# Kernel tuning notes

Measured on AMD Instinct MI355X. Metric: run time of the kernel, lower is better.

## Reference

```python
import jax, jax.numpy as jnp
import numpy as np

N = 20000
E = 320000
IN_C, HID, OUT_C = 128, 64, 32
H12, H3 = 4, 1  # heads for conv1/conv2 and conv3
NEG_SLOPE = 0.2


def _glorot(key, shape):
    fan_in, fan_out = shape[0], shape[-1]
    lim = (6.0 / (fan_in + fan_out)) ** 0.5
    return jax.random.uniform(key, shape, jnp.float32, -lim, lim)


def setup_inputs() -> dict:
    key = jax.random.key(0)
    ks = jax.random.split(key, 16)
    x = jax.random.normal(ks[0], (N, IN_C), jnp.float32)
    edge_index = jax.random.randint(ks[1], (2, E), 0, N, jnp.int64)
    p = {
        'W1': _glorot(ks[2], (IN_C, H12 * HID)),
        'as1': _glorot(ks[3], (H12, HID)), 'ad1': _glorot(ks[4], (H12, HID)),
        'b1': jnp.zeros((HID,), jnp.float32),
        'W2': _glorot(ks[5], (HID, H12 * HID)),
        'as2': _glorot(ks[6], (H12, HID)), 'ad2': _glorot(ks[7], (H12, HID)),
        'b2': jnp.zeros((HID,), jnp.float32),
        'W3': _glorot(ks[8], (HID, H3 * OUT_C)),
        'as3': _glorot(ks[9], (H3, OUT_C)), 'ad3': _glorot(ks[10], (H3, OUT_C)),
        'b3': jnp.zeros((OUT_C,), jnp.float32),
        'Wm': _glorot(ks[11], (OUT_C, OUT_C)), 'bm': jnp.zeros((OUT_C,), jnp.float32),
        'Wv': _glorot(ks[12], (OUT_C, OUT_C)), 'bv': jnp.zeros((OUT_C,), jnp.float32),
    }
    return dict(x=x, edge_index=edge_index, **p)


def gat_layer(x, src, dst, W, a_src, a_dst, b, heads, out_c):
    # x: [N, in_c] -> h: [N, H, C]
    h = (x @ W).reshape(-1, heads, out_c)
    alpha_s = jnp.einsum('nhc,hc->nh', h, a_src)  # [N,H]
    alpha_d = jnp.einsum('nhc,hc->nh', h, a_dst)
    e = jax.nn.leaky_relu(alpha_s[src] + alpha_d[dst], NEG_SLOPE)  # [E',H]
    # segment softmax over incoming edges of each dst node
    m = jax.ops.segment_max(e, dst, num_segments=N)
    p = jnp.exp(e - m[dst])
    s = jax.ops.segment_sum(p, dst, num_segments=N)
    alpha = p / (s[dst] + 1e-16)  # [E',H]
    msg = h[src] * alpha[:, :, None]  # [E',H,C]
    out = jax.ops.segment_sum(msg, dst, num_segments=N)  # [N,H,C]
    return out.mean(axis=1) + b  # concat=False -> mean over heads


def reference(x, edge_index, W1, as1, ad1, b1, W2, as2, ad2, b2,
              W3, as3, ad3, b3, Wm, bm, Wv, bv):
    # PyG GATConv default: add self loops
    loop = jnp.arange(N, dtype=edge_index.dtype)
    src = jnp.concatenate([edge_index[0], loop])
    dst = jnp.concatenate([edge_index[1], loop])

    h = jax.nn.relu(gat_layer(x, src, dst, W1, as1, ad1, b1, H12, HID))
    h = jax.nn.relu(gat_layer(h, src, dst, W2, as2, ad2, b2, H12, HID))
    z = gat_layer(h, src, dst, W3, as3, ad3, b3, H3, OUT_C)

    z_mean = z @ Wm + bm
    z_var = jnp.clip(jnp.exp(z @ Wv + bv), 1e-8, 100.0)
    return (z_mean, z_var, z)
```

## Files before the change

### kernel.cpp

```cpp
#include <hip/hip_runtime.h>
#include <hip/hip_bf16.h>

typedef unsigned short ushortT;
typedef short short8 __attribute__((ext_vector_type(8)));
typedef unsigned short ushort8v __attribute__((ext_vector_type(8)));
typedef float float4v __attribute__((ext_vector_type(4)));

constexpr int Nn   = 20000;
constexpr int Ee   = 320000;
constexpr int EP   = Ee + Nn;
constexpr float NSL = 0.2f;
constexpr int CAP  = 128;

__device__ __forceinline__ float b2f(__hip_bfloat16 v) { return __bfloat162float(v); }
__device__ __forceinline__ float bits2f(unsigned short u) {
    __hip_bfloat16 b; *(unsigned short*)&b = u; return __bfloat162float(b);
}
__device__ __forceinline__ unsigned short f2bits(float v) {
    __hip_bfloat16 b = __float2bfloat16(v); return *(unsigned short*)&b;
}
__device__ __forceinline__ float ldf(const void* p, size_t i, int bf) {
    return bf ? __bfloat162float(((const __hip_bfloat16*)p)[i])
              : ((const float*)p)[i];
}
__device__ __forceinline__ void stf(void* p, size_t i, float v, int bf) {
    if (bf) ((__hip_bfloat16*)p)[i] = __float2bfloat16(v);
    else    ((float*)p)[i] = v;
}

__device__ __forceinline__ int local_bf(const unsigned* __restrict__ xbits, int* c_sh) {
    int c = 0;
    for (int i = threadIdx.x; i < 512; i += 256) {
        unsigned e = (xbits[i] >> 7) & 0xFFu;
        if (e >= 110u && e <= 135u) ++c;
    }
    atomicAdd(c_sh, c);
    __syncthreads();
    return (*c_sh > 384) ? 1 : 0;
}

__global__ void setup_k(const int* __restrict__ ei, const unsigned* __restrict__ xbits,
                        int* __restrict__ eflag, int* __restrict__ fflag,
                        int* __restrict__ cnt,
                        const void* __restrict__ W1, const void* __restrict__ W2,
                        const void* __restrict__ as1, const void* __restrict__ ad1,
                        const void* __restrict__ as2, const void* __restrict__ ad2,
                        ushortT* __restrict__ WT1c, ushortT* __restrict__ WT2c,
                        float* __restrict__ wp1, float* __restrict__ wp2) {
    const int b = blockIdx.x;
    if (b < 79) {
        int gi = b * 256 + threadIdx.x;
        if (gi < Nn) cnt[gi] = 0;
        if (b == 0) {
            __shared__ int bad, c_s;
            if (threadIdx.x == 0) { bad = 0; c_s = 0; }
            __syncthreads();
            for (int i = threadIdx.x; i < 1024; i += 256)
                if (ei[2 * i + 1] != 0) bad = 1;
            int bf = local_bf(xbits, &c_s);
            __syncthreads();
            if (threadIdx.x == 0) {
                *eflag = bad ? 0 : 1;
                *fflag = bf;
            }
        }
        return;
    }
    __shared__ int c_s;
    if (threadIdx.x == 0) c_s = 0;
    __syncthreads();
    const int bf = local_bf(xbits, &c_s);
    if (b < 271) {
        int idx = (b - 79) * 256 + threadIdx.x;
        if (idx < 64 * 512) {
            int jp = idx >> 9, r = idx & 511, hh = r >> 7, k = r & 127;
            WT1c[idx] = f2bits(ldf(W1, (size_t)k * 256 + hh * 64 + jp, bf));
        } else {
            int i2 = idx - 64 * 512;
            int jp = i2 >> 8, r = i2 & 255, hh = r >> 6, k = r & 63;
            WT2c[i2] = f2bits(ldf(W2, (size_t)k * 256 + hh * 64 + jp, bf));
        }
    } else {
        int idx = (b - 271) * 256 + threadIdx.x;
        if (idx < 1024) {
            int sd = idx >> 9, r = idx & 511, hh = r >> 7, k = r & 127;
            const void* av = sd ? ad1 : as1;
            float acc = 0.f;
            for (int c = 0; c < 64; ++c)
                acc = fmaf(ldf(W1, (size_t)k * 256 + hh * 64 + c, bf),
                           ldf(av, hh * 64 + c, bf), acc);
            wp1[idx] = acc;
        } else if (idx < 1536) {
            int i2 = idx - 1024;
            int sd = i2 >> 8, r = i2 & 255, hh = r >> 6, k = r & 63;
            const void* av = sd ? ad2 : as2;
            float acc = 0.f;
            for (int c = 0; c < 64; ++c)
                acc = fmaf(ldf(W2, (size_t)k * 256 + hh * 64 + c, bf),
                           ldf(av, hh * 64 + c, bf), acc);
            wp2[i2] = acc;
        }
    }
}

__device__ __forceinline__ void load_edge(const int* __restrict__ ei, int sh, int e,
                                          int& si, int& di) {
    if (e < Ee) {
        si = ei[(size_t)e << sh];
        di = ei[(size_t)(Ee + e) << sh];
    } else {
        si = di = e - Ee;
    }
}

__global__ void scatter_k(const int* __restrict__ ei, const int* __restrict__ eflag,
                          int* __restrict__ cnt, int* __restrict__ csr) {
    int e = blockIdx.x * 256 + threadIdx.x;
    if (e >= EP) return;
    int sh = *eflag, si, di;
    load_edge(ei, sh, e, si, di);
    int pos = atomicAdd(cnt + di, 1);
    if (pos < CAP) csr[di * CAP + pos] = si;
}

__global__ __launch_bounds__(256) void alpha1_k(const void* __restrict__ xg,
                                                const float* __restrict__ wp1,
                                                ushortT* __restrict__ xb,
                                                float* __restrict__ as_,
                                                float* __restrict__ ad_,
                                                const int* __restrict__ fflag, int N) {
    const int bf = *fflag;
    const int cl = threadIdx.x & 31, g = threadIdx.x >> 5;
    const int n = blockIdx.x * 8 + g;
    if (n >= N) return;
    const int c4 = cl * 4;
    float xv[4];
    if (bf) {
        ushort4 u = *(const ushort4*)((const ushortT*)xg + (size_t)n * 128 + c4);
        xv[0] = bits2f(u.x); xv[1] = bits2f(u.y); xv[2] = bits2f(u.z); xv[3] = bits2f(u.w);
        *(ushort4*)(xb + (size_t)n * 128 + c4) = u;
    } else {
        float4 f = *(const float4*)((const float*)xg + (size_t)n * 128 + c4);
        xv[0] = f.x; xv[1] = f.y; xv[2] = f.z; xv[3] = f.w;
        ushort4 u;
        u.x = f2bits(f.x); u.y = f2bits(f.y); u.z = f2bits(f.z); u.w = f2bits(f.w);
        *(ushort4*)(xb + (size_t)n * 128 + c4) = u;
    }
    float p[8];
#pragma unroll
    for (int j = 0; j < 8; ++j) {
        float4 wv = *(const float4*)(wp1 + j * 128 + c4);
        float t = 0.f;
        t = fmaf(xv[0], wv.x, t);
        t = fmaf(xv[1], wv.y, t);
        t = fmaf(xv[2], wv.z, t);
        t = fmaf(xv[3], wv.w, t);
        p[j] = t;
    }
#pragma unroll
    for (int off = 1; off < 32; off <<= 1) {
#pragma unroll
        for (int j = 0; j < 8; ++j) p[j] += __shfl_xor(p[j], off, 32);
    }
    if (cl == 0) {
        *(float4*)(as_ + (size_t)n * 4) = make_float4(p[0], p[1], p[2], p[3]);
        *(float4*)(ad_ + (size_t)n * 4) = make_float4(p[4], p[5], p[6], p[7]);
    }
}

template <int CIN>
__global__ __launch_bounds__(256) void aggx_k(const int* __restrict__ cnt,
                                              const int* __restrict__ csr,
                                              const float* __restrict__ as_,
                                              const float* __restrict__ ad_,
                                              const ushortT* __restrict__ xb,
                                              ushortT* __restrict__ aggn, int N) {
    constexpr int LPE = CIN / 8;
    constexpr int EPW = 64 / LPE;
    __shared__ float lal[4][CAP][4];
    const int lane = threadIdx.x & 63, seg = threadIdx.x >> 6;
    int d = blockIdx.x * 4 + seg;
    if (d >= N) d = N - 1;
    const int deg = min(cnt[d], CAP);
    const int base = d * CAP;
    const float4 adv = *(const float4*)(ad_ + d * 4);
    const int src0 = (lane < deg) ? csr[base + lane] : 0;
    const int src1 = (64 + lane < deg) ? csr[base + 64 + lane] : 0;
    float s0 = 0, s1 = 0, s2 = 0, s3 = 0;
    if (lane < deg) {
        float4 av = *(const float4*)(as_ + src0 * 4);
        float v0 = av.x + adv.x; v0 = v0 > 0.f ? v0 : NSL * v0; float e0 = __expf(v0);
        float v1 = av.y + adv.y; v1 = v1 > 0.f ? v1 : NSL * v1; float e1 = __expf(v1);
        float v2 = av.z + adv.z; v2 = v2 > 0.f ? v2 : NSL * v2; float e2 = __expf(v2);
        float v3 = av.w + adv.w; v3 = v3 > 0.f ? v3 : NSL * v3; float e3 = __expf(v3);
        s0 += e0; s1 += e1; s2 += e2; s3 += e3;
        *(float4*)(&lal[seg][lane][0]) = make_float4(e0, e1, e2, e3);
    }
    if (64 + lane < deg) {
        float4 av = *(const float4*)(as_ + src1 * 4);
        float v0 = av.x + adv.x; v0 = v0 > 0.f ? v0 : NSL * v0; float e0 = __expf(v0);
        float v1 = av.y + adv.y; v1 = v1 > 0.f ? v1 : NSL * v1; float e1 = __expf(v1);
        float v2 = av.z + adv.z; v2 = v2 > 0.f ? v2 : NSL * v2; float e2 = __expf(v2);
        float v3 = av.w + adv.w; v3 = v3 > 0.f ? v3 : NSL * v3; float e3 = __expf(v3);
        s0 += e0; s1 += e1; s2 += e2; s3 += e3;
        *(float4*)(&lal[seg][64 + lane][0]) = make_float4(e0, e1, e2, e3);
    }
    const int EL = lane / LPE;
    const int c8 = (lane & (LPE - 1)) * 8;
    const float* lal_s = &lal[seg][0][0];
    float a[4][8];
#pragma unroll
    for (int h = 0; h < 4; ++h)
#pragma unroll
        for (int j = 0; j < 8; ++j) a[h][j] = 0.f;

    auto do_edge = [&](int idx, bool valid) {
        int sa = __shfl(src0, idx & 63, 64);
        int sb = __shfl(src1, idx & 63, 64);
        int src = (idx < 64) ? sa : sb;
        int ii = valid ? idx : 0;
        float4 ev = *(const float4*)(lal_s + ii * 4);
        float g = valid ? 1.f : 0.f;
        int off = valid ? src * CIN : 0;
        ushort8v xv = *(const ushort8v*)(xb + (size_t)off + c8);
        float ex0 = ev.x * g, ex1 = ev.y * g, ex2 = ev.z * g, ex3 = ev.w * g;
#pragma unroll
        for (int j = 0; j < 8; ++j) {
            float xf = bits2f(xv[j]);
            a[0][j] = fmaf(ex0, xf, a[0][j]);
            a[1][j] = fmaf(ex1, xf, a[1][j]);
            a[2][j] = fmaf(ex2, xf, a[2][j]);
            a[3][j] = fmaf(ex3, xf, a[3][j]);
        }
    };

    int e = 0;
    for (; e + 2 * EPW <= deg; e += 2 * EPW) {
        do_edge(e + EL, true);
        do_edge(e + EPW + EL, true);
    }
    for (; e < deg; e += EPW) do_edge(e + EL, (e + EL) < deg);

#pragma unroll
    for (int off = 1; off < 64; off <<= 1) {
        s0 += __shfl_xor(s0, off, 64);
        s1 += __shfl_xor(s1, off, 64);
        s2 += __shfl_xor(s2, off, 64);
        s3 += __shfl_xor(s3, off, 64);
    }
#pragma unroll
    for (int h = 0; h < 4; ++h)
#pragma unroll
        for (int j = 0; j < 8; ++j) {
#pragma unroll
            for (int off2 = LPE; off2 < 64; off2 <<= 1)
                a[h][j] += __shfl_xor(a[h][j], off2, 64);
        }
    if (EL == 0) {
        const float i0 = 0.25f / (s0 + 1e-16f);
        const float i1 = 0.25f / (s1 + 1e-16f);
        const float i2 = 0.25f / (s2 + 1e-16f);
        const float i3 = 0.25f / (s3 + 1e-16f);
        ushortT* op = aggn + (size_t)d * (4 * CIN) + c8;
        ushort8v p0, p1, p2, p3;
#pragma unroll
        for (int j = 0; j < 8; ++j) {
            p0[j] = f2bits(a[0][j] * i0);
            p1[j] = f2bits(a[1][j] * i1);
            p2[j] = f2bits(a[2][j] * i2);
            p3[j] = f2bits(a[3][j] * i3);
        }
        *(ushort8v*)(op + 0 * CIN) = p0;
        *(ushort8v*)(op + 1 * CIN) = p1;
        *(ushort8v*)(op + 2 * CIN) = p2;
        *(ushort8v*)(op + 3 * CIN) = p3;
    }
}

template <int K, int NPROJ>
__global__ __launch_bounds__(256) void gemm_cat(const ushortT* __restrict__ aggn,
                                                const ushortT* __restrict__ WTc,
                                                const void* __restrict__ bias,
                                                const float* __restrict__ wp,
                                                ushortT* __restrict__ xout,
                                                float* __restrict__ as_,
                                                float* __restrict__ ad_,
                                                const int* __restrict__ fflag, int N) {
    constexpr int KC = 128, SW = KC + 8, NCH = K / KC;
    const int bf = *fflag;
    __shared__ ushortT wt_s[64 * SW];
    __shared__ ushortT xs[64 * SW];
    __shared__ float wp_s[512];
    const int base = blockIdx.x * 64;
    const int lane = threadIdx.x & 63, w = threadIdx.x >> 6;
    const int ln = lane & 15, quad = lane >> 4;
    float4v acc[4];
#pragma unroll
    for (int T = 0; T < 4; ++T) acc[T] = (float4v){0.f, 0.f, 0.f, 0.f};
    if (NPROJ) {
        for (int i = threadIdx.x; i < NPROJ * 64; i += 256) wp_s[i] = wp[i];
    }
#pragma unroll
    for (int ch = 0; ch < NCH; ++ch) {
        for (int i = threadIdx.x; i < 64 * 16; i += 256) {
            int r = i >> 4, kc = (i & 15) * 8;
            *(short8*)(wt_s + r * SW + kc) =
                *(const short8*)(WTc + (size_t)r * K + ch * KC + kc);
            int node = base + r;
            short8 v = {0, 0, 0, 0, 0, 0, 0, 0};
            if (node < N) v = *(const short8*)(aggn + (size_t)node * K + ch * KC + kc);
            *(short8*)(xs + r * SW + kc) = v;
        }
        __syncthreads();
#pragma unroll
        for (int ks = 0; ks < 4; ++ks) {
            const int kb = ks * 32 + quad * 8;
            const short8 bfr = *(const short8*)(xs + (w * 16 + ln) * SW + kb);
#pragma unroll
            for (int T = 0; T < 4; ++T) {
                const short8 afr = *(const short8*)(wt_s + (T * 16 + ln) * SW + kb);
                acc[T] = __builtin_amdgcn_mfma_f32_16x16x32_bf16(afr, bfr, acc[T], 0, 0, 0);
            }
        }
        __syncthreads();
    }
    const int node = base + w * 16 + ln;
    const bool live = node < N;
    ushortT* on = xout + (size_t)node * 64;
    float p[8];
#pragma unroll
    for (int j = 0; j < 8; ++j) p[j] = 0.f;
#pragma unroll
    for (int T = 0; T < 4; ++T) {
        const int jl = T * 16 + quad * 4;
        ushort4 pk;
        float t0 = fmaxf(acc[T][0] + ldf(bias, jl + 0, bf), 0.f);
        float t1 = fmaxf(acc[T][1] + ldf(bias, jl + 1, bf), 0.f);
        float t2 = fmaxf(acc[T][2] + ldf(bias, jl + 2, bf), 0.f);
        float t3 = fmaxf(acc[T][3] + ldf(bias, jl + 3, bf), 0.f);
        pk.x = f2bits(t0); pk.y = f2bits(t1); pk.z = f2bits(t2); pk.w = f2bits(t3);
        if (live) *(ushort4*)(on + jl) = pk;
        if (NPROJ) {
#pragma unroll
            for (int j = 0; j < 8; ++j) {
                p[j] = fmaf(t0, wp_s[j * 64 + jl + 0], p[j]);
                p[j] = fmaf(t1, wp_s[j * 64 + jl + 1], p[j]);
                p[j] = fmaf(t2, wp_s[j * 64 + jl + 2], p[j]);
                p[j] = fmaf(t3, wp_s[j * 64 + jl + 3], p[j]);
            }
        }
    }
    if (NPROJ) {
#pragma unroll
        for (int j = 0; j < 8; ++j) {
            p[j] += __shfl_xor(p[j], 16, 64);
            p[j] += __shfl_xor(p[j], 32, 64);
        }
        if (quad == 0 && live) {
            *(float4*)(as_ + (size_t)node * 4) = make_float4(p[0], p[1], p[2], p[3]);
            *(float4*)(ad_ + (size_t)node * 4) = make_float4(p[4], p[5], p[6], p[7]);
        }
    }
}

__global__ __launch_bounds__(256) void gemm_small(const ushortT* __restrict__ x,
                                                  const void* __restrict__ W,
                                                  __hip_bfloat16* __restrict__ h,
                                                  const void* __restrict__ avs,
                                                  const void* __restrict__ avd,
                                                  float* __restrict__ as_, float* __restrict__ ad_,
                                                  const int* __restrict__ fflag, int N) {
    constexpr int INC = 64, R = 32, PAD = R + 4;
    const int bf = *fflag;
    __shared__ float xsh[INC * PAD];
    int base = blockIdx.x * R;
    for (int i = threadIdx.x; i < R * INC; i += 256) {
        int rr = i / INC, kk = i - rr * INC;
        int nn = base + rr;
        xsh[kk * PAD + rr] = (nn < N) ? bits2f(x[(size_t)nn * INC + kk]) : 0.0f;
    }
    __syncthreads();
    const int jc = threadIdx.x & 31;
    const int g  = threadIdx.x >> 5;
    float acc[4] = {};
    if (bf) {
        const __hip_bfloat16* Wb = (const __hip_bfloat16*)W;
#pragma unroll 4
        for (int k = 0; k < INC; ++k) {
            float4 xv = *(const float4*)(xsh + k * PAD + g * 4);
            float w = b2f(Wb[k * 32 + jc]);
            acc[0] = fmaf(xv.x, w, acc[0]);
            acc[1] = fmaf(xv.y, w, acc[1]);
            acc[2] = fmaf(xv.z, w, acc[2]);
            acc[3] = fmaf(xv.w, w, acc[3]);
        }
    } else {
        const float* Wf = (const float*)W;
#pragma unroll 4
        for (int k = 0; k < INC; ++k) {
            float4 xv = *(const float4*)(xsh + k * PAD + g * 4);
            float w = Wf[k * 32 + jc];
            acc[0] = fmaf(xv.x, w, acc[0]);
            acc[1] = fmaf(xv.y, w, acc[1]);
            acc[2] = fmaf(xv.z, w, acc[2]);
            acc[3] = fmaf(xv.w, w, acc[3]);
        }
    }
    float avsr = ldf(avs, jc, bf), avdr = ldf(avd, jc, bf);
#pragma unroll
    for (int m = 0; m < 4; ++m) {
        int n = base + g * 4 + m;
        if (n >= N) continue;
        h[(size_t)n * 32 + jc] = __float2bfloat16(acc[m]);
        float t1 = acc[m] * avsr;
        float t2 = acc[m] * avdr;
#pragma unroll
        for (int off = 16; off > 0; off >>= 1) {
            t1 += __shfl_down(t1, off, 32);
            t2 += __shfl_down(t2, off, 32);
        }
        if (jc == 0) { as_[n] = t1; ad_[n] = t2; }
    }
}

__global__ __launch_bounds__(256) void aggr1f_k(const int* __restrict__ cnt,
                                                const int* __restrict__ csr,
                                                const float* __restrict__ as_,
                                                const float* __restrict__ ad_,
                                                const ushortT* __restrict__ h,
                                                const void* __restrict__ b3,
                                                const void* __restrict__ Wm,
                                                const void* __restrict__ bm,
                                                const void* __restrict__ Wv,
                                                const void* __restrict__ bv,
                                                const int* __restrict__ fflag,
                                                void* __restrict__ out, int N) {
    __shared__ float wm_s[1024], wv_s[1024];
    __shared__ float lal[8][CAP];
    __shared__ int   lof[8][CAP];
    const int bf = *fflag;
    for (int i = threadIdx.x; i < 1024; i += 256) {
        wm_s[i] = ldf(Wm, i, bf);
        wv_s[i] = ldf(Wv, i, bf);
    }
    __syncthreads();
    const int c = threadIdx.x & 31, seg = threadIdx.x >> 5;
    const int d = blockIdx.x * 8 + seg;
    if (d >= N) return;
    const int deg = min(cnt[d], CAP);
    const int base = d * CAP;
    const float advd = ad_[d];
    float s = 0;
    for (int i = c; i < deg; i += 32) {
        int src = csr[base + i];
        float v = as_[src] + advd;
        v = v > 0.f ? v : NSL * v;
        float ev = __expf(v);
        s += ev;
        lal[seg][i] = ev;
        lof[seg][i] = src * 32;
    }
    float acc = 0.0f;
    int e = 0;
    for (; e + 4 <= deg; e += 4) {
        float ev0 = lal[seg][e], ev1 = lal[seg][e + 1];
        float ev2 = lal[seg][e + 2], ev3 = lal[seg][e + 3];
        int o0 = lof[seg][e], o1 = lof[seg][e + 1];
        int o2 = lof[seg][e + 2], o3 = lof[seg][e + 3];
        float h0 = bits2f(h[o0 + c]), h1 = bits2f(h[o1 + c]);
        float h2 = bits2f(h[o2 + c]), h3 = bits2f(h[o3 + c]);
        acc = fmaf(ev0, h0, acc);
        acc = fmaf(ev1, h1, acc);
        acc = fmaf(ev2, h2, acc);
        acc = fmaf(ev3, h3, acc);
    }
    for (; e < deg; ++e) acc = fmaf(lal[seg][e], bits2f(h[lof[seg][e] + c]), acc);
#pragma unroll
    for (int off = 1; off < 32; off <<= 1) s += __shfl_xor(s, off, 32);
    const float inv = 1.0f / (s + 1e-16f);
    const float z = inv * acc + ldf(b3, c, bf);
    stf(out, (size_t)2 * N * 32 + (size_t)d * 32 + c, z, bf);
    float sm = ldf(bm, c, bf), sv = ldf(bv, c, bf);
#pragma unroll 8
    for (int k = 0; k < 32; ++k) {
        float zk = __shfl(z, k, 32);
        sm = fmaf(zk, wm_s[k * 32 + c], sm);
        sv = fmaf(zk, wv_s[k * 32 + c], sv);
    }
    float var = __expf(sv);
    var = fminf(fmaxf(var, 1e-8f), 100.0f);
    stf(out, (size_t)d * 32 + c, sm, bf);
    stf(out, (size_t)N * 32 + (size_t)d * 32 + c, var, bf);
}

extern "C" void kernel_launch(void* const* d_in, const int* in_sizes, int n_in,
                              void* d_out, int out_size, void* d_ws, size_t ws_size,
                              hipStream_t stream) {
    const void* x   = d_in[0];
    const int*  ei  = (const int*)d_in[1];
    const void* W1  = d_in[2];
    const void* as1 = d_in[3];
    const void* ad1 = d_in[4];
    const void* b1  = d_in[5];
    const void* W2  = d_in[6];
    const void* as2 = d_in[7];
    const void* ad2 = d_in[8];
    const void* b2  = d_in[9];
    const void* W3  = d_in[10];
    const void* as3 = d_in[11];
    const void* ad3 = d_in[12];
    const void* b3  = d_in[13];
    const void* Wm  = d_in[14];
    const void* bm  = d_in[15];
    const void* Wv  = d_in[16];
    const void* bv  = d_in[17];

    float* ws = (float*)d_ws;
    ushortT* aggn = (ushortT*)ws;
    ushortT* xb   = (ushortT*)(ws + 5120000);
    ushortT* x1b  = (ushortT*)(ws + 6400000);
    ushortT* x2b  = (ushortT*)(ws + 7040000);
    ushortT* h3   = (ushortT*)(ws + 7680000);
    float*  as_   = ws + 8000000;
    float*  ad_   = ws + 8080000;
    ushortT* WT1c = (ushortT*)(ws + 8160000);
    ushortT* WT2c = (ushortT*)(ws + 8176384);
    float*  wp1   = ws + 8184576;
    float*  wp2   = ws + 8185600;
    int*    cnt   = (int*)(ws + 8186112);
    int*    csr   = (int*)(ws + 8206112);
    int*    eflag = (int*)(ws + 10766112);
    int*    fflag = (int*)(ws + 10766113);

    setup_k<<<277, 256, 0, stream>>>(ei, (const unsigned*)x, eflag, fflag, cnt,
                                     W1, W2, as1, ad1, as2, ad2, WT1c, WT2c, wp1, wp2);
    scatter_k<<<(EP + 255) / 256, 256, 0, stream>>>(ei, eflag, cnt, csr);

    alpha1_k<<<2500, 256, 0, stream>>>(x, wp1, xb, as_, ad_, fflag, Nn);
    aggx_k<128><<<5000, 256, 0, stream>>>(cnt, csr, as_, ad_, xb, aggn, Nn);
    gemm_cat<512, 8><<<313, 256, 0, stream>>>(aggn, WT1c, b1, wp2, x1b, as_, ad_, fflag, Nn);

    aggx_k<64><<<5000, 256, 0, stream>>>(cnt, csr, as_, ad_, x1b, aggn, Nn);
    gemm_cat<256, 0><<<313, 256, 0, stream>>>(aggn, WT2c, b2, nullptr, x2b, as_, ad_, fflag, Nn);

    gemm_small<<<625, 256, 0, stream>>>(x2b, W3, (__hip_bfloat16*)h3, as3, ad3, as_, ad_, fflag, Nn);
    aggr1f_k<<<2500, 256, 0, stream>>>(cnt, csr, as_, ad_, h3,
                                       b3, Wm, bm, Wv, bv, fflag, d_out, Nn);
}
```

Measured before the change: 243.1 us.

## Split heads across lanes in aggregation kernels to drop cross-lane reductions

The aggregation kernels now map lanes to (head, channel chunk) instead of (edge, channel chunk). Each lane handles one head, so it keeps 8 accumulators instead of 32 and the large butterfly shuffle reduction over edges disappears (the 64-channel variant still needs one shuffle). The cost is that every lane walks the edges serially, and gathered rows are loaded redundantly by the four head groups, which hurts memory-level parallelism on the per-node loop.

```diff
diff --git a/kernel.cpp b/kernel.cpp
--- a/kernel.cpp
+++ b/kernel.cpp
@@ -168,15 +168,12 @@
     }
 }
 
-template <int CIN>
-__global__ __launch_bounds__(256) void aggx_k(const int* __restrict__ cnt,
-                                              const int* __restrict__ csr,
-                                              const float* __restrict__ as_,
-                                              const float* __restrict__ ad_,
-                                              const ushortT* __restrict__ xb,
-                                              ushortT* __restrict__ aggn, int N) {
-    constexpr int LPE = CIN / 8;
-    constexpr int EPW = 64 / LPE;
+__global__ __launch_bounds__(256) void aggx128_k(const int* __restrict__ cnt,
+                                                 const int* __restrict__ csr,
+                                                 const float* __restrict__ as_,
+                                                 const float* __restrict__ ad_,
+                                                 const ushortT* __restrict__ xb,
+                                                 ushortT* __restrict__ aggn, int N) {
     __shared__ float lal[4][CAP][4];
     const int lane = threadIdx.x & 63, seg = threadIdx.x >> 6;
     int d = blockIdx.x * 4 + seg;
@@ -205,41 +202,28 @@
         s0 += e0; s1 += e1; s2 += e2; s3 += e3;
         *(float4*)(&lal[seg][64 + lane][0]) = make_float4(e0, e1, e2, e3);
     }
-    const int EL = lane / LPE;
-    const int c8 = (lane & (LPE - 1)) * 8;
+    const int q = lane >> 4, c8 = (lane & 15) * 8;
     const float* lal_s = &lal[seg][0][0];
-    float a[4][8];
-#pragma unroll
-    for (int h = 0; h < 4; ++h)
-#pragma unroll
-        for (int j = 0; j < 8; ++j) a[h][j] = 0.f;
-
-    auto do_edge = [&](int idx, bool valid) {
+    float a[8] = {0, 0, 0, 0, 0, 0, 0, 0};
+
+    auto do_edge = [&](int idx) {
         int sa = __shfl(src0, idx & 63, 64);
         int sb = __shfl(src1, idx & 63, 64);
         int src = (idx < 64) ? sa : sb;
-        int ii = valid ? idx : 0;
-        float4 ev = *(const float4*)(lal_s + ii * 4);
-        float g = valid ? 1.f : 0.f;
-        int off = valid ? src * CIN : 0;
-        ushort8v xv = *(const ushort8v*)(xb + (size_t)off + c8);
-        float ex0 = ev.x * g, ex1 = ev.y * g, ex2 = ev.z * g, ex3 = ev.w * g;
-#pragma unroll
-        for (int j = 0; j < 8; ++j) {
-            float xf = bits2f(xv[j]);
-            a[0][j] = fmaf(ex0, xf, a[0][j]);
-            a[1][j] = fmaf(ex1, xf, a[1][j]);
-            a[2][j] = fmaf(ex2, xf, a[2][j]);
-            a[3][j] = fmaf(ex3, xf, a[3][j]);
-        }
+        float ev = lal_s[idx * 4 + q];
+        ushort8v xv = *(const ushort8v*)(xb + (size_t)src * 128 + c8);
+#pragma unroll
+        for (int j = 0; j < 8; ++j) a[j] = fmaf(ev, bits2f(xv[j]), a[j]);
     };
 
     int e = 0;
-    for (; e + 2 * EPW <= deg; e += 2 * EPW) {
-        do_edge(e + EL, true);
-        do_edge(e + EPW + EL, true);
-    }
-    for (; e < deg; e += EPW) do_edge(e + EL, (e + EL) < deg);
+    for (; e + 4 <= deg; e += 4) {
+        do_edge(e);
+        do_edge(e + 1);
+        do_edge(e + 2);
+        do_edge(e + 3);
+    }
+    for (; e < deg; ++e) do_edge(e);
 
 #pragma unroll
     for (int off = 1; off < 64; off <<= 1) {
@@ -248,32 +232,89 @@
         s2 += __shfl_xor(s2, off, 64);
         s3 += __shfl_xor(s3, off, 64);
     }
-#pragma unroll
-    for (int h = 0; h < 4; ++h)
-#pragma unroll
-        for (int j = 0; j < 8; ++j) {
-#pragma unroll
-            for (int off2 = LPE; off2 < 64; off2 <<= 1)
-                a[h][j] += __shfl_xor(a[h][j], off2, 64);
-        }
-    if (EL == 0) {
-        const float i0 = 0.25f / (s0 + 1e-16f);
-        const float i1 = 0.25f / (s1 + 1e-16f);
-        const float i2 = 0.25f / (s2 + 1e-16f);
-        const float i3 = 0.25f / (s3 + 1e-16f);
-        ushortT* op = aggn + (size_t)d * (4 * CIN) + c8;
-        ushort8v p0, p1, p2, p3;
-#pragma unroll
-        for (int j = 0; j < 8; ++j) {
-            p0[j] = f2bits(a[0][j] * i0);
-            p1[j] = f2bits(a[1][j] * i1);
-            p2[j] = f2bits(a[2][j] * i2);
-            p3[j] = f2bits(a[3][j] * i3);
-        }
-        *(ushort8v*)(op + 0 * CIN) = p0;
-        *(ushort8v*)(op + 1 * CIN) = p1;
-        *(ushort8v*)(op + 2 * CIN) = p2;
-        *(ushort8v*)(op + 3 * CIN) = p3;
+    const float sq = (q == 0) ? s0 : (q == 1) ? s1 : (q == 2) ? s2 : s3;
+    const float iq = 0.25f / (sq + 1e-16f);
+    ushort8v p;
+#pragma unroll
+    for (int j = 0; j < 8; ++j) p[j] = f2bits(a[j] * iq);
+    *(ushort8v*)(aggn + (size_t)d * 512 + q * 128 + c8) = p;
+}
+
+__global__ __launch_bounds__(256) void aggx64_k(const int* __restrict__ cnt,
+                                                const int* __restrict__ csr,
+                                                const float* __restrict__ as_,
+                                                const float* __restrict__ ad_,
+                                                const ushortT* __restrict__ xb,
+                                                ushortT* __restrict__ aggn, int N) {
+    __shared__ float lal[4][CAP][4];
+    const int lane = threadIdx.x & 63, seg = threadIdx.x >> 6;
+    int d = blockIdx.x * 4 + seg;
+    if (d >= N) d = N - 1;
+    const int deg = min(cnt[d], CAP);
+    const int base = d * CAP;
+    const float4 adv = *(const float4*)(ad_ + d * 4);
+    const int src0 = (lane < deg) ? csr[base + lane] : 0;
+    const int src1 = (64 + lane < deg) ? csr[base + 64 + lane] : 0;
+    float s0 = 0, s1 = 0, s2 = 0, s3 = 0;
+    if (lane < deg) {
+        float4 av = *(const float4*)(as_ + src0 * 4);
+        float v0 = av.x + adv.x; v0 = v0 > 0.f ? v0 : NSL * v0; float e0 = __expf(v0);
+        float v1 = av.y + adv.y; v1 = v1 > 0.f ? v1 : NSL * v1; float e1 = __expf(v1);
+        float v2 = av.z + adv.z; v2 = v2 > 0.f ? v2 : NSL * v2; float e2 = __expf(v2);
+        float v3 = av.w + adv.w; v3 = v3 > 0.f ? v3 : NSL * v3; float e3 = __expf(v3);
+        s0 += e0; s1 += e1; s2 += e2; s3 += e3;
+        *(float4*)(&lal[seg][lane][0]) = make_float4(e0, e1, e2, e3);
+    }
+    if (64 + lane < deg) {
+        float4 av = *(const float4*)(as_ + src1 * 4);
+        float v0 = av.x + adv.x; v0 = v0 > 0.f ? v0 : NSL * v0; float e0 = __expf(v0);
+        float v1 = av.y + adv.y; v1 = v1 > 0.f ? v1 : NSL * v1; float e1 = __expf(v1);
+        float v2 = av.z + adv.z; v2 = v2 > 0.f ? v2 : NSL * v2; float e2 = __expf(v2);
+        float v3 = av.w + adv.w; v3 = v3 > 0.f ? v3 : NSL * v3; float e3 = __expf(v3);
+        s0 += e0; s1 += e1; s2 += e2; s3 += e3;
+        *(float4*)(&lal[seg][64 + lane][0]) = make_float4(e0, e1, e2, e3);
+    }
+    const int hl = lane >> 5, cl = lane & 31;
+    const int q = cl >> 3, c8 = (cl & 7) * 8;
+    const float* lal_s = &lal[seg][0][0];
+    float a[8] = {0, 0, 0, 0, 0, 0, 0, 0};
+
+    auto do_edge = [&](int idx, bool valid) {
+        int sa = __shfl(src0, idx & 63, 64);
+        int sb = __shfl(src1, idx & 63, 64);
+        int src = (idx < 64) ? sa : sb;
+        float ev = valid ? lal_s[idx * 4 + q] : 0.0f;
+        int off = valid ? src * 64 : 0;
+        ushort8v xv = *(const ushort8v*)(xb + (size_t)off + c8);
+#pragma unroll
+        for (int j = 0; j < 8; ++j) a[j] = fmaf(ev, bits2f(xv[j]), a[j]);
+    };
+
+    int e = 0;
+    for (; e + 8 <= deg; e += 8) {
+        do_edge(e + hl, true);
+        do_edge(e + 2 + hl, true);
+        do_edge(e + 4 + hl, true);
+        do_edge(e + 6 + hl, true);
+    }
+    for (; e < deg; e += 2) do_edge(e + hl, (e + hl) < deg);
+
+#pragma unroll
+    for (int off = 1; off < 64; off <<= 1) {
+        s0 += __shfl_xor(s0, off, 64);
+        s1 += __shfl_xor(s1, off, 64);
+        s2 += __shfl_xor(s2, off, 64);
+        s3 += __shfl_xor(s3, off, 64);
+    }
+#pragma unroll
+    for (int j = 0; j < 8; ++j) a[j] += __shfl_xor(a[j], 32, 64);
+    const float sq = (q == 0) ? s0 : (q == 1) ? s1 : (q == 2) ? s2 : s3;
+    const float iq = 0.25f / (sq + 1e-16f);
+    if (hl == 0) {
+        ushort8v p;
+#pragma unroll
+        for (int j = 0; j < 8; ++j) p[j] = f2bits(a[j] * iq);
+        *(ushort8v*)(aggn + (size_t)d * 256 + q * 64 + c8) = p;
     }
 }
 
@@ -537,10 +578,10 @@
     scatter_k<<<(EP + 255) / 256, 256, 0, stream>>>(ei, eflag, cnt, csr);
 
     alpha1_k<<<2500, 256, 0, stream>>>(x, wp1, xb, as_, ad_, fflag, Nn);
-    aggx_k<128><<<5000, 256, 0, stream>>>(cnt, csr, as_, ad_, xb, aggn, Nn);
+    aggx128_k<<<5000, 256, 0, stream>>>(cnt, csr, as_, ad_, xb, aggn, Nn);
     gemm_cat<512, 8><<<313, 256, 0, stream>>>(aggn, WT1c, b1, wp2, x1b, as_, ad_, fflag, Nn);
 
-    aggx_k<64><<<5000, 256, 0, stream>>>(cnt, csr, as_, ad_, x1b, aggn, Nn);
+    aggx64_k<<<5000, 256, 0, stream>>>(cnt, csr, as_, ad_, x1b, aggn, Nn);
     gemm_cat<256, 0><<<313, 256, 0, stream>>>(aggn, WT2c, b2, nullptr, x2b, as_, ad_, fflag, Nn);
 
     gemm_small<<<625, 256, 0, stream>>>(x2b, W3, (__hip_bfloat16*)h3, as3, ad3, as_, ad_, fflag, Nn);
```

Result: faster. 222.7 us (-8.4%).
